# Kernel optimization log

Measured on AMD Instinct MI355X. Metric: run time of the kernel, lower is better.

Reference implementation:

```python
import jax, jax.numpy as jnp
import numpy as np

EMBED = 1024
HEADS = 16
HEAD_DIM = EMBED // HEADS


def setup_inputs() -> dict:
    key = jax.random.key(0)
    ks = jax.random.split(key, 11)
    B, L, E = 2, 2048, EMBED
    s = 1.0 / np.sqrt(E)
    return {
        "query": jax.random.normal(ks[0], (B, L, E), jnp.float32),
        "key": jax.random.normal(ks[1], (B, L, E), jnp.float32),
        "value": jax.random.normal(ks[2], (B, L, E), jnp.float32),
        "Wq": jax.random.normal(ks[3], (E, E), jnp.float32) * s,
        "bq": jax.random.normal(ks[4], (E,), jnp.float32) * s,
        "Wk": jax.random.normal(ks[5], (E, E), jnp.float32) * s,
        "bk": jax.random.normal(ks[6], (E,), jnp.float32) * s,
        "Wv": jax.random.normal(ks[7], (E, E), jnp.float32) * s,
        "bv": jax.random.normal(ks[8], (E,), jnp.float32) * s,
        "Wo": jax.random.normal(ks[9], (E, E), jnp.float32) * s,
        "bo": jax.random.normal(ks[10], (E,), jnp.float32) * s,
    }


def reference(query, key, value, Wq, bq, Wk, bk, Wv, bv, Wo, bo):
    B, Lq, E = query.shape
    Lk = key.shape[1]
    # Linear projections (torch Linear: x @ W.T + b)
    q = (query @ Wq.T + bq).reshape(B, Lq, HEADS, HEAD_DIM).transpose(0, 2, 1, 3)
    k = (key @ Wk.T + bk).reshape(B, Lk, HEADS, HEAD_DIM).transpose(0, 2, 1, 3)
    v = (value @ Wv.T + bv).reshape(B, Lk, HEADS, HEAD_DIM).transpose(0, 2, 1, 3)
    # NOTE: original scales by sqrt(embed_size), not sqrt(head_dim)
    energy = jnp.einsum("bhqd,bhkd->bhqk", q, k) / jnp.sqrt(jnp.float32(E))
    attn = jax.nn.softmax(energy, axis=-1)
    out = jnp.einsum("bhqk,bhkd->bhqd", attn, v)  # [B,H,Lq,D]
    out = out.transpose(0, 2, 1, 3).reshape(B, Lq, E)
    return out @ Wo.T + bo
```

## Files before the change

### kernel.cpp

```cpp
#include <hip/hip_runtime.h>
#include <hip/hip_bf16.h>


typedef __attribute__((ext_vector_type(4))) float f32x4;
typedef __attribute__((ext_vector_type(16))) float f32x16;
typedef __attribute__((ext_vector_type(8))) short bf16x8;
typedef __attribute__((ext_vector_type(4))) short bf16x4;
typedef __attribute__((ext_vector_type(2))) unsigned int u32x2;

static __device__ __forceinline__ unsigned short f2bf(float f) {
  union { float f; unsigned int u; } a; a.f = f;
  unsigned int u = a.u;
  u += 0x7FFFu + ((u >> 16) & 1u);
  return (unsigned short)(u >> 16);
}

static __device__ __forceinline__ unsigned pack2(float lo, float hi) {
  unsigned a = __float_as_uint(lo) + 0x8000u;
  unsigned b = __float_as_uint(hi) + 0x8000u;
  return __builtin_amdgcn_perm(b, a, 0x07060302);
}

#define AS1(p) ((const __attribute__((address_space(1))) void*)(p))
#define AS3(p) ((__attribute__((address_space(3))) void*)(p))

__global__ __launch_bounds__(256) void cvt_kernel(
    const float* __restrict__ q, const float* __restrict__ k, const float* __restrict__ v,
    const float* __restrict__ wq, const float* __restrict__ wk, const float* __restrict__ wv,
    const float* __restrict__ wo, short* __restrict__ ws) {
  long i = (long)blockIdx.x * 256 + threadIdx.x;
  long e = i * 8;
  const float* src; long off;
  if (e < 12582912) {
    int s = (int)(e >> 22);
    src = s == 0 ? q : (s == 1 ? k : v);
    off = e & 4194303;
  } else {
    long e2 = e - 12582912;
    int s = (int)(e2 >> 20);
    src = s == 0 ? wq : (s == 1 ? wk : (s == 2 ? wv : wo));
    off = e2 & 1048575;
  }
  f32x4 a = *(const f32x4*)(src + off);
  f32x4 b = *(const f32x4*)(src + off + 4);
  bf16x8 o;
  o[0] = (short)f2bf(a[0]); o[1] = (short)f2bf(a[1]);
  o[2] = (short)f2bf(a[2]); o[3] = (short)f2bf(a[3]);
  o[4] = (short)f2bf(b[0]); o[5] = (short)f2bf(b[1]);
  o[6] = (short)f2bf(b[2]); o[7] = (short)f2bf(b[3]);
  *(bf16x8*)(ws + e) = o;
}

__device__ __forceinline__ void gemm_tile(const short* __restrict__ A, const short* __restrict__ B,
                                          int m0, int n0, f32x4 acc[4][4],
                                          short* As, short* Bs) {
  const int t = threadIdx.x;
  const int lane = t & 63, w = t >> 6;
  const int wr = w >> 1, wc = w & 1;
  const int x = lane & 15, g = lane >> 4;
  const int lr = lane >> 3;
  const int lc = ((lane & 7) ^ lr) * 8;
  const int rswz = (x & 7) * 8;

#pragma unroll
  for (int fm = 0; fm < 4; fm++)
#pragma unroll
    for (int fn = 0; fn < 4; fn++)
#pragma unroll
      for (int r = 0; r < 4; r++) acc[fm][fn][r] = 0.0f;

  for (int k0 = 0; k0 < 1024; k0 += 64) {
    __syncthreads();
#pragma unroll
    for (int i = 0; i < 4; i++) {
      int ch = w * 4 + i;
      const short* ga = A + (long)(m0 + ch * 8 + lr) * 1024 + k0 + lc;
      __builtin_amdgcn_global_load_lds(AS1(ga), AS3(As + ch * 512), 16, 0, 0);
      const short* gb = B + (long)(n0 + ch * 8 + lr) * 1024 + k0 + lc;
      __builtin_amdgcn_global_load_lds(AS1(gb), AS3(Bs + ch * 512), 16, 0, 0);
    }
    __syncthreads();
#pragma unroll
    for (int ks = 0; ks < 2; ks++) {
      bf16x8 af[4], bfv[4];
#pragma unroll
      for (int f = 0; f < 4; f++) {
        int c = (ks * 32 + g * 8) ^ rswz;
        af[f]  = *(const bf16x8*)(As + (wr * 64 + f * 16 + x) * 64 + c);
        bfv[f] = *(const bf16x8*)(Bs + (wc * 64 + f * 16 + x) * 64 + c);
      }
#pragma unroll
      for (int fm = 0; fm < 4; fm++)
#pragma unroll
        for (int fn = 0; fn < 4; fn++)
          acc[fm][fn] = __builtin_amdgcn_mfma_f32_16x16x32_bf16(af[fm], bfv[fn], acc[fm][fn], 0, 0, 0);
    }
  }
}

__global__ __launch_bounds__(256) void proj_kernel(
    const short* __restrict__ Xq, const short* __restrict__ Xk, const short* __restrict__ Xv,
    const short* __restrict__ Wq, const short* __restrict__ Wk, const short* __restrict__ Wv,
    const float* __restrict__ bq, const float* __restrict__ bk, const float* __restrict__ bv,
    short* __restrict__ Qo, short* __restrict__ Ko, short* __restrict__ Vto) {
  __shared__ short As[8192], Bs[8192];
  const int z = blockIdx.z;
  const short* A = z == 0 ? Xq : (z == 1 ? Xk : Xv);
  const short* B = z == 0 ? Wq : (z == 1 ? Wk : Wv);
  const float* bias = z == 0 ? bq : (z == 1 ? bk : bv);
  const int m0 = blockIdx.y * 128, n0 = blockIdx.x * 128;
  f32x4 acc[4][4];
  gemm_tile(A, B, m0, n0, acc, As, Bs);

  const int lane = threadIdx.x & 63, w = threadIdx.x >> 6;
  const int wr = w >> 1, wc = w & 1, x = lane & 15, g = lane >> 4;

  if (z == 0) {
    const float scale = 0.04508422002778f;
#pragma unroll
    for (int fn = 0; fn < 4; fn++) {
      int n = n0 + wc * 64 + fn * 16 + x;
      float bb = bias[n];
      int h = n >> 6, d = n & 63;
#pragma unroll
      for (int fm = 0; fm < 4; fm++) {
        int mb = m0 + wr * 64 + fm * 16 + g * 4;
#pragma unroll
        for (int r = 0; r < 4; r++) {
          int m = mb + r;
          int b = m >> 11, l = m & 2047;
          float val = (acc[fm][fn][r] + bb) * scale;
          Qo[((long)((b * 16 + h) * 2048 + l)) * 64 + d] = (short)f2bf(val);
        }
      }
    }
  } else if (z == 1) {
#pragma unroll
    for (int fn = 0; fn < 4; fn++) {
      int n = n0 + wc * 64 + fn * 16 + x;
      float bb = bias[n];
      int h = n >> 6, d = n & 63;
#pragma unroll
      for (int fm = 0; fm < 4; fm++) {
        int mb = m0 + wr * 64 + fm * 16 + g * 4;
#pragma unroll
        for (int r = 0; r < 4; r++) {
          int m = mb + r;
          int b = m >> 11, kv = m & 2047;
          int ds = d ^ ((kv & 7) << 3);
          Ko[((long)((b * 16 + h) * 2048 + kv)) * 64 + ds] = (short)f2bf(acc[fm][fn][r] + bb);
        }
      }
    }
  } else {
#pragma unroll
    for (int fn = 0; fn < 4; fn++) {
      int n = n0 + wc * 64 + fn * 16 + x;
      float bb = bias[n];
      int h = n >> 6, d = n & 63;
#pragma unroll
      for (int fm = 0; fm < 4; fm++) {
        int mb = m0 + wr * 64 + fm * 16 + g * 4;
        int b = mb >> 11, kvb = mb & 2047;
        bf16x4 pk;
#pragma unroll
        for (int r = 0; r < 4; r++) pk[r] = (short)f2bf(acc[fm][fn][r] + bb);
        int kvs = (kvb & ~63) | ((kvb & 63) ^ ((d & 7) << 3));
        *(bf16x4*)(Vto + ((long)((b * 16 + h) * 64 + d)) * 2048 + kvs) = pk;
      }
    }
  }
}

__global__ __launch_bounds__(256, 2) void attn_kernel(
    const short* __restrict__ Qg, const short* __restrict__ Kg,
    const short* __restrict__ Vtg, short* __restrict__ Og) {
  __shared__ __align__(16) short Kl[2][8192];
  __shared__ __align__(16) short Vl[2][8192];
  __shared__ __align__(16) short Pl[4][32][64];
  const int t = threadIdx.x, w = t >> 6, lane = t & 63;
  const int col = lane & 31, hi = lane >> 5;
  const int bh = blockIdx.y;
  const int q0 = blockIdx.x * 128 + w * 32;
  const long hb = (long)bh * 2048 * 64;
  const int swz = (col & 7) * 8;

  bf16x8 qf[4];
#pragma unroll
  for (int ksl = 0; ksl < 4; ksl++)
    qf[ksl] = *(const bf16x8*)(Qg + hb + (long)(q0 + col) * 64 + ksl * 16 + hi * 8);

  f32x16 o0, o1;
#pragma unroll
  for (int i = 0; i < 16; i++) { o0[i] = 0.0f; o1[i] = 0.0f; }
  float l_r = 0.0f;

  auto stage = [&](int buf, int kv0) {
#pragma unroll
    for (int it = 0; it < 4; it++) {
      int cb = it * 256 + w * 64;
      const short* gk = Kg + hb + (long)kv0 * 64 + (cb + lane) * 8;
      __builtin_amdgcn_global_load_lds(AS1(gk), AS3(&Kl[buf][cb * 8]), 16, 0, 0);
      int c = cb + lane;
      const short* gv = Vtg + hb + (long)(c >> 4) * 2048 + kv0 + (c & 15) * 8;
      __builtin_amdgcn_global_load_lds(AS1(gv), AS3(&Vl[buf][cb * 8]), 16, 0, 0);
    }
  };

  auto qkt = [&](int buf, int st, f32x16& r0, f32x16& r1) {
#pragma unroll
    for (int i = 0; i < 16; i++) { r0[i] = 0.0f; r1[i] = 0.0f; }
    __builtin_amdgcn_s_setprio(1);
#pragma unroll
    for (int ksl = 0; ksl < 4; ksl++) {
      int dcol = (ksl * 16 + hi * 8) ^ swz;
      bf16x8 a0 = *(const bf16x8*)(&Kl[buf][(st * 64 + col) * 64 + dcol]);
      bf16x8 a1 = *(const bf16x8*)(&Kl[buf][(st * 64 + col + 32) * 64 + dcol]);
      r0 = __builtin_amdgcn_mfma_f32_32x32x16_bf16(a0, qf[ksl], r0, 0, 0, 0);
      r1 = __builtin_amdgcn_mfma_f32_32x32x16_bf16(a1, qf[ksl], r1, 0, 0, 0);
    }
    __builtin_amdgcn_s_setprio(0);
  };

  auto smpv = [&](int buf, int st, f32x16& s0, f32x16& s1) {
#pragma unroll
    for (int i = 0; i < 16; i++) { s0[i] = __builtin_amdgcn_exp2f(s0[i]); }
#pragma unroll
    for (int i = 0; i < 16; i++) { s1[i] = __builtin_amdgcn_exp2f(s1[i]); }
    {
      float a0 = s0[0] + s0[1], a1 = s0[2] + s0[3], a2 = s0[4] + s0[5], a3 = s0[6] + s0[7];
      float a4 = s0[8] + s0[9], a5 = s0[10] + s0[11], a6 = s0[12] + s0[13], a7 = s0[14] + s0[15];
      float b0 = s1[0] + s1[1], b1 = s1[2] + s1[3], b2 = s1[4] + s1[5], b3 = s1[6] + s1[7];
      float b4 = s1[8] + s1[9], b5 = s1[10] + s1[11], b6 = s1[12] + s1[13], b7 = s1[14] + s1[15];
      float c0 = a0 + a1, c1 = a2 + a3, c2 = a4 + a5, c3 = a6 + a7;
      float c4 = b0 + b1, c5 = b2 + b3, c6 = b4 + b5, c7 = b6 + b7;
      float d0 = c0 + c1, d1 = c2 + c3, d2 = c4 + c5, d3 = c6 + c7;
      l_r += (d0 + d1) + (d2 + d3);
    }
#pragma unroll
    for (int j = 0; j < 4; j++) {
      u32x2 p0, p1;
      p0[0] = pack2(s0[4 * j + 0], s0[4 * j + 1]);
      p0[1] = pack2(s0[4 * j + 2], s0[4 * j + 3]);
      int kv = 8 * j + 4 * hi;
      *(u32x2*)&Pl[w][col][kv ^ swz] = p0;
      p1[0] = pack2(s1[4 * j + 0], s1[4 * j + 1]);
      p1[1] = pack2(s1[4 * j + 2], s1[4 * j + 3]);
      *(u32x2*)&Pl[w][col][(32 + kv) ^ swz] = p1;
    }
    __builtin_amdgcn_s_setprio(1);
#pragma unroll
    for (int KS = 0; KS < 4; KS++) {
      const int vcol = (KS * 16 + hi * 8) ^ swz;
      bf16x8 pb  = *(const bf16x8*)&Pl[w][col][vcol];
      bf16x8 vb0 = *(const bf16x8*)(&Vl[buf][col * 128 + st * 64 + vcol]);
      bf16x8 vb1 = *(const bf16x8*)(&Vl[buf][(col + 32) * 128 + st * 64 + vcol]);
      o0 = __builtin_amdgcn_mfma_f32_32x32x16_bf16(vb0, pb, o0, 0, 0, 0);
      o1 = __builtin_amdgcn_mfma_f32_32x32x16_bf16(vb1, pb, o1, 0, 0, 0);
    }
    __builtin_amdgcn_s_setprio(0);
  };

  stage(0, 0);
  __syncthreads();

  f32x16 cur0, cur1, nxt0, nxt1;
  qkt(0, 0, cur0, cur1);
  for (int ti = 0; ti < 16; ti++) {
    const int buf = ti & 1;
    if (ti < 15) stage(buf ^ 1, (ti + 1) * 128);
    qkt(buf, 1, nxt0, nxt1);
    smpv(buf, 0, cur0, cur1);
    smpv(buf, 1, nxt0, nxt1);
    __syncthreads();
    if (ti < 15) qkt(buf ^ 1, 0, cur0, cur1);
  }

  const float l_tot = l_r + __shfl_xor(l_r, 32);
  const float inv = 1.0f / l_tot;
  const int b = bh >> 4, h = bh & 15;
  const long base = ((long)(b * 2048 + q0 + col) * 16 + h) * 64;
#pragma unroll
  for (int dh = 0; dh < 2; dh++) {
#pragma unroll
    for (int g2 = 0; g2 < 4; g2++) {
      float x0 = (dh ? o1[g2 * 4 + 0] : o0[g2 * 4 + 0]) * inv;
      float x1 = (dh ? o1[g2 * 4 + 1] : o0[g2 * 4 + 1]) * inv;
      float x2 = (dh ? o1[g2 * 4 + 2] : o0[g2 * 4 + 2]) * inv;
      float x3 = (dh ? o1[g2 * 4 + 3] : o0[g2 * 4 + 3]) * inv;
      u32x2 rr;
      rr[0] = (unsigned)f2bf(x0) | ((unsigned)f2bf(x1) << 16);
      rr[1] = (unsigned)f2bf(x2) | ((unsigned)f2bf(x3) << 16);
      int d = dh * 32 + g2 * 8 + hi * 4;
      *(u32x2*)(Og + base + d) = rr;
    }
  }
}

__global__ __launch_bounds__(256) void out_kernel(
    const short* __restrict__ O, const short* __restrict__ Wo,
    const float* __restrict__ bo, float* __restrict__ out) {
  __shared__ short As[8192], Bs[8192];
  const int m0 = blockIdx.y * 128, n0 = blockIdx.x * 128;
  f32x4 acc[4][4];
  gemm_tile(O, Wo, m0, n0, acc, As, Bs);
  const int lane = threadIdx.x & 63, w = threadIdx.x >> 6;
  const int wr = w >> 1, wc = w & 1, x = lane & 15, g = lane >> 4;
#pragma unroll
  for (int fn = 0; fn < 4; fn++) {
    int n = n0 + wc * 64 + fn * 16 + x;
    float bb = bo[n];
#pragma unroll
    for (int fm = 0; fm < 4; fm++) {
      int mb = m0 + wr * 64 + fm * 16 + g * 4;
#pragma unroll
      for (int r = 0; r < 4; r++)
        out[(long)(mb + r) * 1024 + n] = acc[fm][fn][r] + bb;
    }
  }
}

extern "C" void kernel_launch(void* const* d_in, const int* in_sizes, int n_in,
                              void* d_out, int out_size, void* d_ws, size_t ws_size,
                              hipStream_t stream) {
  const float* q  = (const float*)d_in[0];
  const float* k  = (const float*)d_in[1];
  const float* v  = (const float*)d_in[2];
  const float* wq = (const float*)d_in[3];
  const float* bq = (const float*)d_in[4];
  const float* wk = (const float*)d_in[5];
  const float* bk = (const float*)d_in[6];
  const float* wv = (const float*)d_in[7];
  const float* bv = (const float*)d_in[8];
  const float* wo = (const float*)d_in[9];
  const float* bo = (const float*)d_in[10];

  short* ws  = (short*)d_ws;
  short* Xq  = ws;
  short* Xk  = Xq + 4194304;
  short* Xv  = Xk + 4194304;
  short* Wqb = Xv + 4194304;
  short* Wkb = Wqb + 1048576;
  short* Wvb = Wkb + 1048576;
  short* Wob = Wvb + 1048576;
  short* Qb  = Wob + 1048576;
  short* Kb  = Qb + 4194304;
  short* Vtb = Kb + 4194304;
  short* Ob  = Vtb + 4194304;

  cvt_kernel<<<8192, 256, 0, stream>>>(q, k, v, wq, wk, wv, wo, ws);
  dim3 gp(8, 32, 3);
  proj_kernel<<<gp, 256, 0, stream>>>(Xq, Xk, Xv, Wqb, Wkb, Wvb, bq, bk, bv, Qb, Kb, Vtb);
  dim3 ga(16, 32);
  attn_kernel<<<ga, 256, 0, stream>>>(Qb, Kb, Vtb, Ob);
  dim3 gf(8, 32);
  out_kernel<<<gf, 256, 0, stream>>>(Ob, Wob, bo, (float*)d_out);
}
```

Measured before the change: 136.5 us.

## Pass P to PV MFMA through permlane32 swaps instead of LDS round-trip

Replaces the per-wave LDS staging buffer for the softmax probabilities with register-level cross-half exchanges using permlane32_swap, building the PV MFMA B-operand directly from the QK^T accumulators. This removes LDS writes and reads and frees 16KB of shared memory per block. It also drops the software pipelining that overlapped the next QK^T with the current softmax/PV, so each sub-tile now runs QK^T, exp, then PV in sequence, which may expose MFMA latency. The final row-sum reduction also switches from shfl_xor to the same swap helper.

```diff
diff --git a/kernel.cpp b/kernel.cpp
--- a/kernel.cpp
+++ b/kernel.cpp
@@ -19,6 +19,11 @@
   unsigned a = __float_as_uint(lo) + 0x8000u;
   unsigned b = __float_as_uint(hi) + 0x8000u;
   return __builtin_amdgcn_perm(b, a, 0x07060302);
+}
+
+static __device__ __forceinline__ unsigned xchg32(unsigned x) {
+  u32x2 r = __builtin_amdgcn_permlane32_swap(x, x, false, false);
+  return x ^ r[0] ^ r[1];
 }
 
 #define AS1(p) ((const __attribute__((address_space(1))) void*)(p))
@@ -177,7 +182,6 @@
     const short* __restrict__ Vtg, short* __restrict__ Og) {
   __shared__ __align__(16) short Kl[2][8192];
   __shared__ __align__(16) short Vl[2][8192];
-  __shared__ __align__(16) short Pl[4][32][64];
   const int t = threadIdx.x, w = t >> 6, lane = t & 63;
   const int col = lane & 31, hi = lane >> 5;
   const int bh = blockIdx.y;
@@ -207,76 +211,76 @@
     }
   };
 
-  auto qkt = [&](int buf, int st, f32x16& r0, f32x16& r1) {
-#pragma unroll
-    for (int i = 0; i < 16; i++) { r0[i] = 0.0f; r1[i] = 0.0f; }
-    __builtin_amdgcn_s_setprio(1);
-#pragma unroll
-    for (int ksl = 0; ksl < 4; ksl++) {
-      int dcol = (ksl * 16 + hi * 8) ^ swz;
-      bf16x8 a0 = *(const bf16x8*)(&Kl[buf][(st * 64 + col) * 64 + dcol]);
-      bf16x8 a1 = *(const bf16x8*)(&Kl[buf][(st * 64 + col + 32) * 64 + dcol]);
-      r0 = __builtin_amdgcn_mfma_f32_32x32x16_bf16(a0, qf[ksl], r0, 0, 0, 0);
-      r1 = __builtin_amdgcn_mfma_f32_32x32x16_bf16(a1, qf[ksl], r1, 0, 0, 0);
-    }
-    __builtin_amdgcn_s_setprio(0);
-  };
-
-  auto smpv = [&](int buf, int st, f32x16& s0, f32x16& s1) {
-#pragma unroll
-    for (int i = 0; i < 16; i++) { s0[i] = __builtin_amdgcn_exp2f(s0[i]); }
-#pragma unroll
-    for (int i = 0; i < 16; i++) { s1[i] = __builtin_amdgcn_exp2f(s1[i]); }
-    {
-      float a0 = s0[0] + s0[1], a1 = s0[2] + s0[3], a2 = s0[4] + s0[5], a3 = s0[6] + s0[7];
-      float a4 = s0[8] + s0[9], a5 = s0[10] + s0[11], a6 = s0[12] + s0[13], a7 = s0[14] + s0[15];
-      float b0 = s1[0] + s1[1], b1 = s1[2] + s1[3], b2 = s1[4] + s1[5], b3 = s1[6] + s1[7];
-      float b4 = s1[8] + s1[9], b5 = s1[10] + s1[11], b6 = s1[12] + s1[13], b7 = s1[14] + s1[15];
-      float c0 = a0 + a1, c1 = a2 + a3, c2 = a4 + a5, c3 = a6 + a7;
-      float c4 = b0 + b1, c5 = b2 + b3, c6 = b4 + b5, c7 = b6 + b7;
-      float d0 = c0 + c1, d1 = c2 + c3, d2 = c4 + c5, d3 = c6 + c7;
-      l_r += (d0 + d1) + (d2 + d3);
-    }
-#pragma unroll
-    for (int j = 0; j < 4; j++) {
-      u32x2 p0, p1;
-      p0[0] = pack2(s0[4 * j + 0], s0[4 * j + 1]);
-      p0[1] = pack2(s0[4 * j + 2], s0[4 * j + 3]);
-      int kv = 8 * j + 4 * hi;
-      *(u32x2*)&Pl[w][col][kv ^ swz] = p0;
-      p1[0] = pack2(s1[4 * j + 0], s1[4 * j + 1]);
-      p1[1] = pack2(s1[4 * j + 2], s1[4 * j + 3]);
-      *(u32x2*)&Pl[w][col][(32 + kv) ^ swz] = p1;
-    }
-    __builtin_amdgcn_s_setprio(1);
-#pragma unroll
-    for (int KS = 0; KS < 4; KS++) {
-      const int vcol = (KS * 16 + hi * 8) ^ swz;
-      bf16x8 pb  = *(const bf16x8*)&Pl[w][col][vcol];
-      bf16x8 vb0 = *(const bf16x8*)(&Vl[buf][col * 128 + st * 64 + vcol]);
-      bf16x8 vb1 = *(const bf16x8*)(&Vl[buf][(col + 32) * 128 + st * 64 + vcol]);
-      o0 = __builtin_amdgcn_mfma_f32_32x32x16_bf16(vb0, pb, o0, 0, 0, 0);
-      o1 = __builtin_amdgcn_mfma_f32_32x32x16_bf16(vb1, pb, o1, 0, 0, 0);
-    }
-    __builtin_amdgcn_s_setprio(0);
-  };
-
   stage(0, 0);
   __syncthreads();
 
-  f32x16 cur0, cur1, nxt0, nxt1;
-  qkt(0, 0, cur0, cur1);
   for (int ti = 0; ti < 16; ti++) {
     const int buf = ti & 1;
     if (ti < 15) stage(buf ^ 1, (ti + 1) * 128);
-    qkt(buf, 1, nxt0, nxt1);
-    smpv(buf, 0, cur0, cur1);
-    smpv(buf, 1, nxt0, nxt1);
+
+#pragma unroll
+    for (int st = 0; st < 2; st++) {
+      f32x16 s0, s1;
+#pragma unroll
+      for (int i = 0; i < 16; i++) { s0[i] = 0.0f; s1[i] = 0.0f; }
+      __builtin_amdgcn_s_setprio(1);
+#pragma unroll
+      for (int ksl = 0; ksl < 4; ksl++) {
+        int dcol = (ksl * 16 + hi * 8) ^ swz;
+        bf16x8 a0 = *(const bf16x8*)(&Kl[buf][(st * 64 + col) * 64 + dcol]);
+        bf16x8 a1 = *(const bf16x8*)(&Kl[buf][(st * 64 + col + 32) * 64 + dcol]);
+        s0 = __builtin_amdgcn_mfma_f32_32x32x16_bf16(a0, qf[ksl], s0, 0, 0, 0);
+        s1 = __builtin_amdgcn_mfma_f32_32x32x16_bf16(a1, qf[ksl], s1, 0, 0, 0);
+      }
+      __builtin_amdgcn_s_setprio(0);
+
+#pragma unroll
+      for (int i = 0; i < 16; i++) { s0[i] = __builtin_amdgcn_exp2f(s0[i]); }
+#pragma unroll
+      for (int i = 0; i < 16; i++) { s1[i] = __builtin_amdgcn_exp2f(s1[i]); }
+      {
+        float a0 = s0[0] + s0[1], a1 = s0[2] + s0[3], a2 = s0[4] + s0[5], a3 = s0[6] + s0[7];
+        float a4 = s0[8] + s0[9], a5 = s0[10] + s0[11], a6 = s0[12] + s0[13], a7 = s0[14] + s0[15];
+        float b0 = s1[0] + s1[1], b1 = s1[2] + s1[3], b2 = s1[4] + s1[5], b3 = s1[6] + s1[7];
+        float b4 = s1[8] + s1[9], b5 = s1[10] + s1[11], b6 = s1[12] + s1[13], b7 = s1[14] + s1[15];
+        float c0 = a0 + a1, c1 = a2 + a3, c2 = a4 + a5, c3 = a6 + a7;
+        float c4 = b0 + b1, c5 = b2 + b3, c6 = b4 + b5, c7 = b6 + b7;
+        float d0 = c0 + c1, d1 = c2 + c3, d2 = c4 + c5, d3 = c6 + c7;
+        l_r += (d0 + d1) + (d2 + d3);
+      }
+
+#define PVSTEP(SEL, KS)                                                       \
+      {                                                                       \
+        const int qo = 4 * (((KS) & 1) * 2 + hi);                             \
+        const int qx = 4 * (((KS) & 1) * 2 + (hi ^ 1));                       \
+        unsigned own0 = pack2(SEL[qo + 0], SEL[qo + 1]);                      \
+        unsigned own1 = pack2(SEL[qo + 2], SEL[qo + 3]);                      \
+        unsigned out0 = pack2(SEL[qx + 0], SEL[qx + 1]);                      \
+        unsigned out1 = pack2(SEL[qx + 2], SEL[qx + 3]);                      \
+        unsigned r0 = xchg32(out0);                                           \
+        unsigned r1 = xchg32(out1);                                           \
+        union { unsigned u[4]; bf16x8 v; } pb;                                \
+        pb.u[0] = hi ? r0 : own0; pb.u[1] = hi ? r1 : own1;                   \
+        pb.u[2] = hi ? own0 : r0; pb.u[3] = hi ? own1 : r1;                   \
+        const int vcol = ((KS) * 16 + hi * 8) ^ swz;                          \
+        bf16x8 vb0 = *(const bf16x8*)(&Vl[buf][col * 128 + st * 64 + vcol]);  \
+        bf16x8 vb1 = *(const bf16x8*)(&Vl[buf][(col + 32) * 128 + st * 64 + vcol]); \
+        __builtin_amdgcn_s_setprio(1);                                        \
+        o0 = __builtin_amdgcn_mfma_f32_32x32x16_bf16(vb0, pb.v, o0, 0, 0, 0); \
+        o1 = __builtin_amdgcn_mfma_f32_32x32x16_bf16(vb1, pb.v, o1, 0, 0, 0); \
+        __builtin_amdgcn_s_setprio(0);                                        \
+      }
+      PVSTEP(s0, 0)
+      PVSTEP(s0, 1)
+      PVSTEP(s1, 2)
+      PVSTEP(s1, 3)
+#undef PVSTEP
+    }
+
     __syncthreads();
-    if (ti < 15) qkt(buf ^ 1, 0, cur0, cur1);
-  }
-
-  const float l_tot = l_r + __shfl_xor(l_r, 32);
+  }
+
+  const float l_tot = l_r + __uint_as_float(xchg32(__float_as_uint(l_r)));
   const float inv = 1.0f / l_tot;
   const int b = bh >> 4, h = bh & 15;
   const long base = ((long)(b * 2048 + q0 + col) * 16 + h) * 64;
```

After: 313.0 us. +129.3%, slower.
